# Kernel tuning notes

Measured on AMD Instinct MI355X. Metric: run time of the kernel, lower is better.

The kernel has to match this reference:

```python
import jax, jax.numpy as jnp
import numpy as np
import math

N_HEAD = 16
N_EMBD = 2048

def setup_inputs() -> dict:
    key = jax.random.key(0)
    k1, k2, k3, k4, k5 = jax.random.split(key, 5)
    B, T, C = 4, 2048, N_EMBD
    x = jax.random.normal(k1, (B, T, C), dtype=jnp.float32)
    # torch Linear stores weight [out,in]; we store [in,out] for x @ W
    s_attn = 1.0 / math.sqrt(C)
    w_attn = jax.random.normal(k2, (C, 3 * C), dtype=jnp.float32) * s_attn
    b_attn = jnp.zeros((3 * C,), dtype=jnp.float32)
    w_proj = jax.random.normal(k3, (C, C), dtype=jnp.float32) * s_attn
    b_proj = jnp.zeros((C,), dtype=jnp.float32)
    return {"x": x, "w_attn": w_attn, "b_attn": b_attn,
            "w_proj": w_proj, "b_proj": b_proj}

def reference(x, w_attn, b_attn, w_proj, b_proj):
    B, T, C = x.shape
    H = N_HEAD
    D = C // H
    qkv = x @ w_attn + b_attn                      # [B,T,3C]
    q, k, v = jnp.split(qkv, 3, axis=2)
    q = q.reshape(B, T, H, D).transpose(0, 2, 1, 3)  # [B,H,T,D]
    k = k.reshape(B, T, H, D).transpose(0, 2, 1, 3)
    v = v.reshape(B, T, H, D).transpose(0, 2, 1, 3)
    scale = 1.0 / math.sqrt(D)
    att = jnp.einsum('bhqd,bhkd->bhqk', q, k) * scale  # [B,H,T,T]
    causal = jnp.tril(jnp.ones((T, T), dtype=bool))    # mask slice bias[:, :, FULL_T-T:FULL_T, :FULL_T] with FULL_T==T
    att = jnp.where(causal[None, None], att, -jnp.inf)
    att = jax.nn.softmax(att.astype(jnp.float32), axis=-1).astype(att.dtype)
    y = jnp.einsum('bhqk,bhkd->bhqd', att, v)          # [B,H,T,D]
    y = y.transpose(0, 2, 1, 3).reshape(B, T, C)
    return y @ w_proj + b_proj
```

## Files before the change

kernel.cpp:

```cpp
#include <hip/hip_runtime.h>
#include <hip/hip_bf16.h>

#define NB 4
#define TT 2048
#define CC 2048
#define HH 16
#define DD 128

typedef short bvec8 __attribute__((ext_vector_type(8)));
typedef float fvec4 __attribute__((ext_vector_type(4)));

__device__ __forceinline__ void gload16(const void* g, void* l) {
  __builtin_amdgcn_global_load_lds(
      (__attribute__((address_space(1))) void*)g,
      (__attribute__((address_space(3))) void*)l, 16, 0, 0);
}

__device__ __forceinline__ unsigned short f2bf(float f) {
  union { float f; unsigned int u; } x; x.f = f;
  unsigned int u = x.u;
  return (unsigned short)((u + 0x7FFFu + ((u >> 16) & 1u)) >> 16);
}

__device__ __forceinline__ fvec4 mfma16(bvec8 a, bvec8 b, fvec4 c) {
  return __builtin_amdgcn_mfma_f32_16x16x32_bf16(a, b, c, 0, 0, 0);
}

#define KSC (0.08838834764831845f * 1.4426950408889634f)

__global__ __launch_bounds__(256) void k_cvt(const float* __restrict__ in,
                                             unsigned short* __restrict__ out, int n4) {
  int i = blockIdx.x * 256 + threadIdx.x;
  if (i >= n4) return;
  float4 v = ((const float4*)in)[i];
  ushort4 o;
  o.x = f2bf(v.x); o.y = f2bf(v.y); o.z = f2bf(v.z); o.w = f2bf(v.w);
  ((ushort4*)out)[i] = o;
}

__global__ __launch_bounds__(256) void k_transpose(const float* __restrict__ in,
                                                   unsigned short* __restrict__ out,
                                                   int R, int Cn) {
  __shared__ unsigned short tile[64][65];
  int tC = blockIdx.x * 64, tR = blockIdx.y * 64;
  int t = threadIdx.x;
  for (int i = 0; i < 16; i++) {
    int idx = t + i * 256; int r = idx >> 6, c = idx & 63;
    tile[r][c] = f2bf(in[(size_t)(tR + r) * Cn + tC + c]);
  }
  __syncthreads();
  for (int i = 0; i < 16; i++) {
    int idx = t + i * 256; int r = idx >> 6, c = idx & 63;
    out[(size_t)(tC + r) * R + tR + c] = tile[c][r];
  }
}

template <int EPI>
__global__ __launch_bounds__(512, 2) void k_gemm8(
    const unsigned short* __restrict__ A,
    const unsigned short* __restrict__ Bt,
    const float* __restrict__ bias,
    unsigned short* __restrict__ qk,
    unsigned short* __restrict__ vt,
    float* __restrict__ out) {
  const int K = CC;
  const int nt = K / 64;
  __shared__ unsigned short sm[2][32768];

  int tid = threadIdx.x;
  int wid = tid >> 6, ln = tid & 63, gl = ln >> 4, lo = ln & 15;
  int wr = wid >> 2, wc = wid & 3;

  unsigned nx = gridDim.x;
  unsigned orig = blockIdx.y * nx + blockIdx.x;
  unsigned cpx = (nx * gridDim.y) >> 3;
  unsigned wg = (orig & 7) * cpx + (orig >> 3);
  int m0 = (int)(wg / nx) * 256, n0 = (int)(wg % nx) * 256;

  auto stageA = [&](int buf, int half, int kt) {
#pragma unroll
    for (int j = 0; j < 2; j++) {
      int c = j * 512 + tid;
      int r = c >> 3;
      int kc = (c & 7) ^ (r & 7);
      gload16(A + (size_t)(m0 + half * 128 + r) * K + kt * 64 + kc * 8,
              &sm[buf][(size_t)(half * 1024 + c) * 8]);
    }
  };
  auto stageB = [&](int buf, int half, int kt) {
#pragma unroll
    for (int j = 0; j < 2; j++) {
      int c = j * 512 + tid;
      int r = c >> 3;
      int kc = (c & 7) ^ (r & 7);
      gload16(Bt + (size_t)(n0 + half * 128 + r) * K + kt * 64 + kc * 8,
              &sm[buf][16384 + (size_t)(half * 1024 + c) * 8]);
    }
  };

#define AFRAG(buf, mi, ks) \
  (*(const bvec8*)&sm[buf][(((wr * 128 + (mi) * 16 + lo) * 8) + ((((ks) * 4 + gl)) ^ (lo & 7))) * 8])
#define BFRAG(buf, nj, ks) \
  (*(const bvec8*)&sm[buf][16384 + (((wc * 64 + (nj) * 16 + lo) * 8) + ((((ks) * 4 + gl)) ^ (lo & 7))) * 8])

  fvec4 acc[8][4];
  fvec4 zero = {0.f, 0.f, 0.f, 0.f};
#pragma unroll
  for (int i = 0; i < 8; i++)
#pragma unroll
    for (int j = 0; j < 4; j++) acc[i][j] = zero;

  stageA(0, 0, 0); stageA(0, 1, 0); stageB(0, 0, 0); stageB(0, 1, 0);
  stageA(1, 0, 1); stageA(1, 1, 1);
  asm volatile("s_waitcnt vmcnt(4)" ::: "memory");
  __builtin_amdgcn_sched_barrier(0);
  __builtin_amdgcn_s_barrier();

  for (int t = 0; t < nt; t++) {
    int cur = t & 1;
    bvec8 a0[4], a1[4], a2[4], a3[4], b0[4], b1[4];

#pragma unroll
    for (int mi = 0; mi < 4; mi++) a0[mi] = AFRAG(cur, mi, 0);
#pragma unroll
    for (int nj = 0; nj < 4; nj++) b0[nj] = BFRAG(cur, nj, 0);
    if (t + 1 < nt) stageB(cur ^ 1, 0, t + 1);
    __builtin_amdgcn_s_barrier();
    asm volatile("s_waitcnt lgkmcnt(0)" ::: "memory");
    __builtin_amdgcn_sched_barrier(0);
    __builtin_amdgcn_s_setprio(1);
#pragma unroll
    for (int mi = 0; mi < 4; mi++)
#pragma unroll
      for (int nj = 0; nj < 4; nj++) acc[mi][nj] = mfma16(a0[mi], b0[nj], acc[mi][nj]);
    __builtin_amdgcn_s_setprio(0);
    __builtin_amdgcn_s_barrier();

#pragma unroll
    for (int mi = 0; mi < 4; mi++) a1[mi] = AFRAG(cur, mi + 4, 0);
#pragma unroll
    for (int nj = 0; nj < 4; nj++) b1[nj] = BFRAG(cur, nj, 1);
    if (t + 1 < nt) stageB(cur ^ 1, 1, t + 1);
    __builtin_amdgcn_s_barrier();
    asm volatile("s_waitcnt lgkmcnt(0)" ::: "memory");
    __builtin_amdgcn_sched_barrier(0);
    __builtin_amdgcn_s_setprio(1);
#pragma unroll
    for (int mi = 0; mi < 4; mi++)
#pragma unroll
      for (int nj = 0; nj < 4; nj++) acc[mi + 4][nj] = mfma16(a1[mi], b0[nj], acc[mi + 4][nj]);
    __builtin_amdgcn_s_setprio(0);
    __builtin_amdgcn_s_barrier();

#pragma unroll
    for (int mi = 0; mi < 4; mi++) a2[mi] = AFRAG(cur, mi, 1);
#pragma unroll
    for (int mi = 0; mi < 4; mi++) a3[mi] = AFRAG(cur, mi + 4, 1);
    __builtin_amdgcn_s_barrier();
    asm volatile("s_waitcnt lgkmcnt(0)" ::: "memory");
    __builtin_amdgcn_sched_barrier(0);
    __builtin_amdgcn_s_setprio(1);
#pragma unroll
    for (int mi = 0; mi < 4; mi++)
#pragma unroll
      for (int nj = 0; nj < 4; nj++) acc[mi][nj] = mfma16(a2[mi], b1[nj], acc[mi][nj]);
    __builtin_amdgcn_s_setprio(0);
    __builtin_amdgcn_s_barrier();

    if (t + 2 < nt) { stageA(cur, 0, t + 2); stageA(cur, 1, t + 2); }
    if (t + 2 < nt) {
      asm volatile("s_waitcnt vmcnt(4)" ::: "memory");
    } else {
      asm volatile("s_waitcnt vmcnt(0)" ::: "memory");
    }
    __builtin_amdgcn_sched_barrier(0);
    __builtin_amdgcn_s_barrier();
    __builtin_amdgcn_s_setprio(1);
#pragma unroll
    for (int mi = 0; mi < 4; mi++)
#pragma unroll
      for (int nj = 0; nj < 4; nj++) acc[mi + 4][nj] = mfma16(a3[mi], b1[nj], acc[mi + 4][nj]);
    __builtin_amdgcn_s_setprio(0);
    __builtin_amdgcn_s_barrier();
  }

  if (EPI == 0) {
#pragma unroll
    for (int nj = 0; nj < 4; nj++) {
      int n = n0 + wc * 64 + nj * 16 + lo;
      float bn = bias[n];
      int s = n >> 11, hh = (n >> 7) & 15, d = n & 127;
      float mulv = (s == 1) ? KSC : 1.0f;
#pragma unroll
      for (int mi = 0; mi < 8; mi++) {
        int mb = m0 + wr * 128 + mi * 16 + gl * 4;
        int b = mb >> 11, t0 = mb & 2047;
        if (s < 2) {
          size_t base = ((((size_t)s * NB + b) * HH + hh) * TT) * DD;
#pragma unroll
          for (int r = 0; r < 4; r++)
            qk[base + (size_t)(t0 + r) * DD + d] = f2bf((acc[mi][nj][r] + bn) * mulv);
        } else {
          size_t base = (((size_t)b * HH + hh) * DD + d) * TT + t0;
          ushort4 o;
          o.x = f2bf(acc[mi][nj][0] + bn);
          o.y = f2bf(acc[mi][nj][1] + bn);
          o.z = f2bf(acc[mi][nj][2] + bn);
          o.w = f2bf(acc[mi][nj][3] + bn);
          *(ushort4*)&vt[base] = o;
        }
      }
    }
  } else {
#pragma unroll
    for (int nj = 0; nj < 4; nj++) {
      int n = n0 + wc * 64 + nj * 16 + lo;
      float bn = bias[n];
#pragma unroll
      for (int mi = 0; mi < 8; mi++) {
        int m = m0 + wr * 128 + mi * 16 + gl * 4;
#pragma unroll
        for (int r = 0; r < 4; r++) out[(size_t)(m + r) * CC + n] = acc[mi][nj][r] + bn;
      }
    }
  }
#undef AFRAG
#undef BFRAG
}

__global__ __launch_bounds__(256) void k_attn(
    const unsigned short* __restrict__ qk,
    const unsigned short* __restrict__ vt,
    unsigned short* __restrict__ yb) {
  __shared__ unsigned short Ks[64 * 128];
  __shared__ unsigned short Vs[128 * 64];
  __shared__ unsigned short Ps[4][16 * 64];
  int tid = threadIdx.x, wid = tid >> 6, ln = tid & 63;
  int gl = ln >> 4, lo = ln & 15;
  int qp = blockIdx.x & 15;
  int bh = blockIdx.x >> 4;
  int b = bh >> 4, h = bh & 15;
  const unsigned short* Q  = qk + (((size_t)b * HH + h) * TT) * DD;
  const unsigned short* Kg = qk + ((((size_t)NB + b) * HH + h) * TT) * DD;
  const unsigned short* Vg = vt + (((size_t)b * HH + h) * DD) * TT;
  fvec4 zero = {0.f, 0.f, 0.f, 0.f};

  for (int pass = 0; pass < 2; pass++) {
    int qt = pass ? (31 - qp) : qp;
    int q0w = qt * 64 + wid * 16;

    bvec8 qf[4];
#pragma unroll
    for (int ks = 0; ks < 4; ks++)
      qf[ks] = *(const bvec8*)(Q + (size_t)(q0w + lo) * DD + ks * 32 + gl * 8);

    fvec4 oacc[8];
#pragma unroll
    for (int i = 0; i < 8; i++) oacc[i] = zero;
    float mrun[4] = {-1e30f, -1e30f, -1e30f, -1e30f};
    float lrun[4] = {0.f, 0.f, 0.f, 0.f};

    int ntiles = qt + 1;
    for (int it = 0; it < ntiles; it++) {
      int k0 = it * 64;
#pragma unroll
      for (int j = 0; j < 4; j++) {
        int c = j * 256 + tid;
        int r = c >> 4, cc = c & 15;
        gload16(Kg + (size_t)(k0 + r) * DD + ((cc ^ (r & 7)) * 8), &Ks[(j * 256 + wid * 64) * 8]);
      }
#pragma unroll
      for (int j = 0; j < 4; j++) {
        int c = j * 256 + tid;
        int r = c >> 3, cc = c & 7;
        gload16(Vg + (size_t)r * TT + k0 + ((cc ^ (r & 7)) * 8), &Vs[(j * 256 + wid * 64) * 8]);
      }
      __syncthreads();

      fvec4 sa[4];
#pragma unroll
      for (int fn = 0; fn < 4; fn++) {
        fvec4 s = zero;
#pragma unroll
        for (int ks = 0; ks < 4; ks++) {
          int r = fn * 16 + lo;
          int cd = ks * 4 + gl;
          bvec8 kf = *(const bvec8*)&Ks[(r * 16 + (cd ^ (r & 7))) * 8];
          s = mfma16(qf[ks], kf, s);
        }
        sa[fn] = s;
      }

      float p[4][4], mx[4];
      bool lastt = (it == qt);
#pragma unroll
      for (int r = 0; r < 4; r++) {
        int qrow = q0w + gl * 4 + r;
        float m = -1e30f;
        if (lastt) {
#pragma unroll
          for (int fn = 0; fn < 4; fn++) {
            int kkg = k0 + fn * 16 + lo;
            float v = (kkg <= qrow) ? sa[fn][r] : -1e30f;
            p[fn][r] = v;
            m = fmaxf(m, v);
          }
        } else {
#pragma unroll
          for (int fn = 0; fn < 4; fn++) {
            float v = sa[fn][r];
            p[fn][r] = v;
            m = fmaxf(m, v);
          }
        }
#pragma unroll
        for (int dlt = 1; dlt < 16; dlt <<= 1) m = fmaxf(m, __shfl_xor(m, dlt));
        mx[r] = m;
      }
      bool grow = !__all((mx[0] <= mrun[0] + 8.f) && (mx[1] <= mrun[1] + 8.f) &&
                         (mx[2] <= mrun[2] + 8.f) && (mx[3] <= mrun[3] + 8.f));
      if (grow) {
#pragma unroll
        for (int r = 0; r < 4; r++) {
          float mnew = fmaxf(mrun[r], mx[r]);
          float corr = exp2f(mrun[r] - mnew);
          mrun[r] = mnew;
          lrun[r] *= corr;
#pragma unroll
          for (int fd = 0; fd < 8; fd++) oacc[fd][r] *= corr;
        }
      }
#pragma unroll
      for (int r = 0; r < 4; r++) {
        float ls = 0.f;
#pragma unroll
        for (int fn = 0; fn < 4; fn++) {
          float pv = exp2f(p[fn][r] - mrun[r]);
          p[fn][r] = pv;
          ls += pv;
        }
#pragma unroll
        for (int dlt = 1; dlt < 16; dlt <<= 1) ls += __shfl_xor(ls, dlt);
        lrun[r] += ls;
      }

#pragma unroll
      for (int fn = 0; fn < 4; fn++)
#pragma unroll
        for (int r = 0; r < 4; r++) {
          int qr = gl * 4 + r;
          int kc = fn * 16 + lo;
          Ps[wid][(qr * 8 + (((kc >> 3) ^ (qr & 7)))) * 8 + (kc & 7)] = f2bf(p[fn][r]);
        }

#pragma unroll
      for (int ks2 = 0; ks2 < 2; ks2++) {
        bvec8 pf = *(const bvec8*)&Ps[wid][(lo * 8 + ((ks2 * 4 + gl) ^ (lo & 7))) * 8];
#pragma unroll
        for (int fd = 0; fd < 8; fd++) {
          int rd = fd * 16 + lo;
          int ck = ks2 * 4 + gl;
          bvec8 vf = *(const bvec8*)&Vs[(rd * 8 + (ck ^ (rd & 7))) * 8];
          oacc[fd] = mfma16(pf, vf, oacc[fd]);
        }
      }
      __syncthreads();
    }

#pragma unroll
    for (int r = 0; r < 4; r++) {
      int qrow = q0w + gl * 4 + r;
      float inv = 1.f / lrun[r];
#pragma unroll
      for (int fd = 0; fd < 8; fd++) {
        int d = fd * 16 + lo;
        yb[((size_t)b * TT + qrow) * CC + h * DD + d] = f2bf(oacc[fd][r] * inv);
      }
    }
  }
}

extern "C" void kernel_launch(void* const* d_in, const int* in_sizes, int n_in,
                              void* d_out, int out_size, void* d_ws, size_t ws_size,
                              hipStream_t stream) {
  const float* x      = (const float*)d_in[0];
  const float* w_attn = (const float*)d_in[1];
  const float* b_attn = (const float*)d_in[2];
  const float* w_proj = (const float*)d_in[3];
  const float* b_proj = (const float*)d_in[4];
  float* out = (float*)d_out;

  char* ws = (char*)d_ws;
  unsigned short* xb    = (unsigned short*)(ws);
  unsigned short* wab_t = (unsigned short*)(ws + 33554432);
  unsigned short* wpb_t = (unsigned short*)(ws + 58720256);
  unsigned short* qkws  = (unsigned short*)(ws + 67108864);
  unsigned short* vtws  = (unsigned short*)(ws + 134217728);
  unsigned short* ybws  = (unsigned short*)(ws + 167772160);

  hipLaunchKernelGGL(k_cvt, dim3(16384), dim3(256), 0, stream, x, xb, 4194304);
  hipLaunchKernelGGL(k_transpose, dim3(96, 32), dim3(256), 0, stream, w_attn, wab_t, 2048, 6144);
  hipLaunchKernelGGL(k_transpose, dim3(32, 32), dim3(256), 0, stream, w_proj, wpb_t, 2048, 2048);
  hipLaunchKernelGGL((k_gemm8<0>), dim3(24, 32), dim3(512), 0, stream,
                     xb, wab_t, b_attn, qkws, vtws, (float*)nullptr);
  hipLaunchKernelGGL(k_attn, dim3(1024), dim3(256), 0, stream, qkws, vtws, ybws);
  hipLaunchKernelGGL((k_gemm8<1>), dim3(8, 32), dim3(512), 0, stream,
                     ybws, wpb_t, b_proj, (unsigned short*)nullptr, (unsigned short*)nullptr, out);
}
```

Baseline: 509.4 us.

## Double-buffer K/V tiles in attention, retile V layout, defer row-sum reductions

Adds double-buffered LDS for K and V so the next tile's global_load_lds is issued before computing the current tile, with one waitcnt and barrier per iteration instead of two syncthreads. V^T is now written in a blocked [t/8][d][8] layout so each 16-byte load is contiguous and LDS reads need no swizzle. The per-tile row-sum shuffle reduction is moved to the end, and the max reduction now runs only when some lane's local max exceeds the threshold. LDS use doubles, which may lower occupancy, and the unswizzled V reads may cause bank conflicts.

After: 480.4 us. 5.7% less time.

```diff
diff --git a/kernel.cpp b/kernel.cpp
--- a/kernel.cpp
+++ b/kernel.cpp
@@ -201,7 +201,7 @@
           for (int r = 0; r < 4; r++)
             qk[base + (size_t)(t0 + r) * DD + d] = f2bf((acc[mi][nj][r] + bn) * mulv);
         } else {
-          size_t base = (((size_t)b * HH + hh) * DD + d) * TT + t0;
+          size_t base = ((((size_t)b * HH + hh) * (TT / 8) + (t0 >> 3)) * DD + d) * 8 + (t0 & 7);
           ushort4 o;
           o.x = f2bf(acc[mi][nj][0] + bn);
           o.y = f2bf(acc[mi][nj][1] + bn);
@@ -232,9 +232,9 @@
     const unsigned short* __restrict__ qk,
     const unsigned short* __restrict__ vt,
     unsigned short* __restrict__ yb) {
-  __shared__ unsigned short Ks[64 * 128];
-  __shared__ unsigned short Vs[128 * 64];
-  __shared__ unsigned short Ps[4][16 * 64];
+  __shared__ unsigned short Ks[2][8192];
+  __shared__ unsigned short Vs[2][8192];
+  __shared__ unsigned short Ps[4][1024];
   int tid = threadIdx.x, wid = tid >> 6, ln = tid & 63;
   int gl = ln >> 4, lo = ln & 15;
   int qp = blockIdx.x & 15;
@@ -242,8 +242,24 @@
   int b = bh >> 4, h = bh & 15;
   const unsigned short* Q  = qk + (((size_t)b * HH + h) * TT) * DD;
   const unsigned short* Kg = qk + ((((size_t)NB + b) * HH + h) * TT) * DD;
-  const unsigned short* Vg = vt + (((size_t)b * HH + h) * DD) * TT;
+  const unsigned short* Vg = vt + (((size_t)b * HH + h) * (TT / 8)) * DD * 8;
   fvec4 zero = {0.f, 0.f, 0.f, 0.f};
+
+  auto stage = [&](int buf, int it) {
+    int k0 = it * 64;
+#pragma unroll
+    for (int j = 0; j < 4; j++) {
+      int c = j * 256 + tid;
+      int r = c >> 4, cc = c & 15;
+      gload16(Kg + (size_t)(k0 + r) * DD + ((cc ^ (r & 7)) * 8), &Ks[buf][(j * 256 + wid * 64) * 8]);
+    }
+#pragma unroll
+    for (int j = 0; j < 4; j++) {
+      int c = j * 256 + tid;
+      int cc = c >> 7, d = c & 127;
+      gload16(Vg + ((size_t)(k0 / 8 + cc) * DD + d) * 8, &Vs[buf][(j * 256 + wid * 64) * 8]);
+    }
+  };
 
   for (int pass = 0; pass < 2; pass++) {
     int qt = pass ? (31 - qp) : qp;
@@ -261,21 +277,16 @@
     float lrun[4] = {0.f, 0.f, 0.f, 0.f};
 
     int ntiles = qt + 1;
+    stage(0, 0);
+    asm volatile("s_waitcnt vmcnt(0)" ::: "memory");
+    __builtin_amdgcn_sched_barrier(0);
+    __builtin_amdgcn_s_barrier();
+    __builtin_amdgcn_sched_barrier(0);
+
     for (int it = 0; it < ntiles; it++) {
+      int cur = it & 1;
       int k0 = it * 64;
-#pragma unroll
-      for (int j = 0; j < 4; j++) {
-        int c = j * 256 + tid;
-        int r = c >> 4, cc = c & 15;
-        gload16(Kg + (size_t)(k0 + r) * DD + ((cc ^ (r & 7)) * 8), &Ks[(j * 256 + wid * 64) * 8]);
-      }
-#pragma unroll
-      for (int j = 0; j < 4; j++) {
-        int c = j * 256 + tid;
-        int r = c >> 3, cc = c & 7;
-        gload16(Vg + (size_t)r * TT + k0 + ((cc ^ (r & 7)) * 8), &Vs[(j * 256 + wid * 64) * 8]);
-      }
-      __syncthreads();
+      if (it + 1 < ntiles) stage(cur ^ 1, it + 1);
 
       fvec4 sa[4];
 #pragma unroll
@@ -285,13 +296,13 @@
         for (int ks = 0; ks < 4; ks++) {
           int r = fn * 16 + lo;
           int cd = ks * 4 + gl;
-          bvec8 kf = *(const bvec8*)&Ks[(r * 16 + (cd ^ (r & 7))) * 8];
+          bvec8 kf = *(const bvec8*)&Ks[cur][(r * 16 + (cd ^ (r & 7))) * 8];
           s = mfma16(qf[ks], kf, s);
         }
         sa[fn] = s;
       }
 
-      float p[4][4], mx[4];
+      float p[4][4], mxl[4];
       bool lastt = (it == qt);
 #pragma unroll
       for (int r = 0; r < 4; r++) {
@@ -313,16 +324,17 @@
             m = fmaxf(m, v);
           }
         }
-#pragma unroll
-        for (int dlt = 1; dlt < 16; dlt <<= 1) m = fmaxf(m, __shfl_xor(m, dlt));
-        mx[r] = m;
-      }
-      bool grow = !__all((mx[0] <= mrun[0] + 8.f) && (mx[1] <= mrun[1] + 8.f) &&
-                         (mx[2] <= mrun[2] + 8.f) && (mx[3] <= mrun[3] + 8.f));
-      if (grow) {
+        mxl[r] = m;
+      }
+      bool c = (mxl[0] > mrun[0] + 8.f) || (mxl[1] > mrun[1] + 8.f) ||
+               (mxl[2] > mrun[2] + 8.f) || (mxl[3] > mrun[3] + 8.f);
+      if (__any(c)) {
 #pragma unroll
         for (int r = 0; r < 4; r++) {
-          float mnew = fmaxf(mrun[r], mx[r]);
+          float m = mxl[r];
+#pragma unroll
+          for (int dlt = 1; dlt < 16; dlt <<= 1) m = fmaxf(m, __shfl_xor(m, dlt));
+          float mnew = fmaxf(mrun[r], m);
           float corr = exp2f(mrun[r] - mnew);
           mrun[r] = mnew;
           lrun[r] *= corr;
@@ -332,16 +344,12 @@
       }
 #pragma unroll
       for (int r = 0; r < 4; r++) {
-        float ls = 0.f;
 #pragma unroll
         for (int fn = 0; fn < 4; fn++) {
           float pv = exp2f(p[fn][r] - mrun[r]);
           p[fn][r] = pv;
-          ls += pv;
-        }
-#pragma unroll
-        for (int dlt = 1; dlt < 16; dlt <<= 1) ls += __shfl_xor(ls, dlt);
-        lrun[r] += ls;
+          lrun[r] += pv;
+        }
       }
 
 #pragma unroll
@@ -358,19 +366,24 @@
         bvec8 pf = *(const bvec8*)&Ps[wid][(lo * 8 + ((ks2 * 4 + gl) ^ (lo & 7))) * 8];
 #pragma unroll
         for (int fd = 0; fd < 8; fd++) {
-          int rd = fd * 16 + lo;
-          int ck = ks2 * 4 + gl;
-          bvec8 vf = *(const bvec8*)&Vs[(rd * 8 + (ck ^ (rd & 7))) * 8];
+          bvec8 vf = *(const bvec8*)&Vs[cur][((ks2 * 4 + gl) * 128 + fd * 16 + lo) * 8];
           oacc[fd] = mfma16(pf, vf, oacc[fd]);
         }
       }
-      __syncthreads();
+
+      asm volatile("s_waitcnt vmcnt(0)" ::: "memory");
+      __builtin_amdgcn_sched_barrier(0);
+      __builtin_amdgcn_s_barrier();
+      __builtin_amdgcn_sched_barrier(0);
     }
 
 #pragma unroll
     for (int r = 0; r < 4; r++) {
+      float l = lrun[r];
+#pragma unroll
+      for (int dlt = 1; dlt < 16; dlt <<= 1) l += __shfl_xor(l, dlt);
       int qrow = q0w + gl * 4 + r;
-      float inv = 1.f / lrun[r];
+      float inv = 1.f / l;
 #pragma unroll
       for (int fd = 0; fd < 8; fd++) {
         int d = fd * 16 + lo;
```
